# Performance work log

Hardware: AMD Instinct MI355X
Metric: run time of the kernel (lower is better)

The kernel has to match this reference:

```python
import jax, jax.numpy as jnp
import numpy as np

B, S, HID, NH = 2, 2048, 2048, 16
NOPE, ROPE, VD = 128, 64, 128
QKD = NOPE + ROPE          # 192
KVR, QR = 512, 1536
EPS = 1e-6
SCALE = QKD ** (-0.5)


def rmsnorm(x, gamma, eps=EPS):
    return x * jax.lax.rsqrt(jnp.mean(x * x, axis=-1, keepdims=True) + eps) * gamma


def rotate_half(x):
    h = x.shape[-1] // 2
    return jnp.concatenate([-x[..., h:], x[..., :h]], axis=-1)


def apply_rope(x, cos, sin):
    # x: [b, h, s, d_rope]; cos/sin: [b, 1, s, d_rope]
    return x * cos + rotate_half(x) * sin


def setup_inputs() -> dict:
    key = jax.random.key(0)
    ks = jax.random.split(key, 8)
    hidden_states = jax.random.normal(ks[0], (B, S, HID), dtype=jnp.float32)
    # Standard NeoX-style rotary tables for the decoupled RoPE sub-dim
    pos = jnp.arange(S, dtype=jnp.float32)
    inv_freq = 1.0 / (10000.0 ** (jnp.arange(0, ROPE, 2, dtype=jnp.float32) / ROPE))
    freqs = pos[:, None] * inv_freq[None, :]              # [S, ROPE/2]
    emb = jnp.concatenate([freqs, freqs], axis=-1)        # [S, ROPE]
    cos = jnp.broadcast_to(jnp.cos(emb)[None], (B, S, ROPE)).astype(jnp.float32)
    sin = jnp.broadcast_to(jnp.sin(emb)[None], (B, S, ROPE)).astype(jnp.float32)
    std = 0.02
    Wq_down = jax.random.normal(ks[1], (QR, HID), dtype=jnp.float32) * std
    q_gamma = jnp.ones((QR,), dtype=jnp.float32)
    Wq_up = jax.random.normal(ks[2], (NH * QKD, QR), dtype=jnp.float32) * std
    Wkv_down = jax.random.normal(ks[3], (KVR + ROPE, HID), dtype=jnp.float32) * std
    kv_gamma = jnp.ones((KVR,), dtype=jnp.float32)
    Wkv_up = jax.random.normal(ks[4], (NH * (NOPE + VD), KVR), dtype=jnp.float32) * std
    Wo = jax.random.normal(ks[5], (HID, NH * VD), dtype=jnp.float32) * std
    return {
        "hidden_states": hidden_states, "cos": cos, "sin": sin,
        "Wq_down": Wq_down, "q_gamma": q_gamma, "Wq_up": Wq_up,
        "Wkv_down": Wkv_down, "kv_gamma": kv_gamma, "Wkv_up": Wkv_up,
        "Wo": Wo,
    }


def reference(hidden_states, cos, sin, Wq_down, q_gamma, Wq_up,
              Wkv_down, kv_gamma, Wkv_up, Wo):
    b, s, _ = hidden_states.shape
    cos4 = cos[:, None, :, :]  # [b,1,s,ROPE]
    sin4 = sin[:, None, :, :]

    # Q path: low-rank down -> RMSNorm -> up
    q_lat = rmsnorm(hidden_states @ Wq_down.T, q_gamma)            # [b,s,QR]
    q = (q_lat @ Wq_up.T).reshape(b, s, NH, QKD).transpose(0, 2, 1, 3)  # [b,h,s,QKD]
    q_nope, q_rope = q[..., :NOPE], q[..., NOPE:]
    q_rope = apply_rope(q_rope, cos4, sin4)
    q = jnp.concatenate([q_nope, q_rope], axis=-1)                 # [b,h,s,QKD]

    # KV path: joint down-proj -> split latent / shared rope key
    kv = hidden_states @ Wkv_down.T                                # [b,s,KVR+ROPE]
    c_kv, k_rope = kv[..., :KVR], kv[..., KVR:]
    c_kv = rmsnorm(c_kv, kv_gamma)
    kvx = (c_kv @ Wkv_up.T).reshape(b, s, NH, NOPE + VD).transpose(0, 2, 1, 3)
    k_nope, v = kvx[..., :NOPE], kvx[..., NOPE:]                   # [b,h,s,*]

    # Shared rope key, broadcast to all heads, rotated
    k_rope = apply_rope(k_rope[:, None, :, :], cos4, sin4)         # [b,1,s,ROPE]
    k_rope = jnp.broadcast_to(k_rope, (b, NH, s, ROPE))
    k = jnp.concatenate([k_nope, k_rope], axis=-1)                 # [b,h,s,QKD]

    # SDPA with causal mask (V zero-padded to QKD in the original -> identical
    # to using V directly and slicing, so we use V directly)
    scores = jnp.einsum('bhqd,bhkd->bhqk', q, k) * SCALE           # [b,h,s,s]
    causal = jnp.tril(jnp.ones((s, s), dtype=bool))
    scores = jnp.where(causal[None, None], scores, jnp.finfo(scores.dtype).min)
    attn = jax.nn.softmax(scores, axis=-1)
    out = jnp.einsum('bhqk,bhkd->bhqd', attn, v)                   # [b,h,s,VD]
    out = out.transpose(0, 2, 1, 3).reshape(b, s, NH * VD)
    return out @ Wo.T                                              # [b,s,HID]
```

## Files before the change

kernel.cpp:

```cpp
#include <hip/hip_runtime.h>
#include <math.h>

#define SCALE_F 0.0721687836487032f

typedef __attribute__((ext_vector_type(8))) short bf16x8;
typedef __attribute__((ext_vector_type(4))) float f32x4;

static __device__ __forceinline__ short f2bf(float f) {
  unsigned u = __float_as_uint(f);
  u += 0x7fffu + ((u >> 16) & 1u);
  return (short)(u >> 16);
}

static __device__ __forceinline__ void gl_lds16(const void* g, void* l) {
  __builtin_amdgcn_global_load_lds((const __attribute__((address_space(1))) void*)g,
                                   (__attribute__((address_space(3))) void*)l, 16, 0, 0);
}

template <int MODE>
__global__ __launch_bounds__(256) void gemm_mfma(
    const short* __restrict__ A, const short* __restrict__ W,
    void* __restrict__ Cout, int N, int K,
    const float* __restrict__ cosb, const float* __restrict__ sinb,
    short* __restrict__ out2)
{
  __shared__ __align__(16) short As[128 * 32];
  __shared__ __align__(16) short Ws[128 * 32];
  const int tid = threadIdx.x;
  const int lane = tid & 63;
  const int quad = lane >> 4, n16 = lane & 15;
  const int bm = blockIdx.y * 128, bn = blockIdx.x * 128;
  const int wr = ((tid >> 6) >> 1) * 64, wc = ((tid >> 6) & 1) * 64;

  f32x4 acc[4][4];
  #pragma unroll
  for (int i = 0; i < 4; ++i)
    #pragma unroll
    for (int j = 0; j < 4; ++j) acc[i][j] = (f32x4){0.f, 0.f, 0.f, 0.f};

  const int r0 = tid >> 2, c0 = (tid & 3) * 8;
  const short* a0p = A + (size_t)(bm + r0) * K + c0;
  const short* a1p = A + (size_t)(bm + 64 + r0) * K + c0;
  const short* w0p = W + (size_t)(bn + r0) * K + c0;
  const short* w1p = W + (size_t)(bn + 64 + r0) * K + c0;
  short* asd0 = &As[tid * 8];
  short* asd1 = &As[2048 + tid * 8];
  short* wsd0 = &Ws[tid * 8];
  short* wsd1 = &Ws[2048 + tid * 8];

  for (int k0 = 0; k0 < K; k0 += 32) {
    gl_lds16(a0p, asd0);
    gl_lds16(a1p, asd1);
    gl_lds16(w0p, wsd0);
    gl_lds16(w1p, wsd1);
    a0p += 32; a1p += 32; w0p += 32; w1p += 32;
    __syncthreads();

    bf16x8 af[4], wf[4];
    #pragma unroll
    for (int i = 0; i < 4; ++i) {
      af[i] = *(const bf16x8*)&As[(wr + i * 16 + n16) * 32 + quad * 8];
      wf[i] = *(const bf16x8*)&Ws[(wc + i * 16 + n16) * 32 + quad * 8];
    }
    #pragma unroll
    for (int i = 0; i < 4; ++i)
      #pragma unroll
      for (int j = 0; j < 4; ++j)
        acc[i][j] = __builtin_amdgcn_mfma_f32_16x16x32_bf16(af[i], wf[j], acc[i][j], 0, 0, 0);
    __syncthreads();
  }

  if (MODE == 0) {
    #pragma unroll
    for (int i = 0; i < 4; ++i)
      #pragma unroll
      for (int r = 0; r < 4; ++r) {
        size_t row = (size_t)(bm + wr + i * 16 + quad * 4 + r);
        #pragma unroll
        for (int j = 0; j < 4; ++j)
          ((float*)Cout)[row * N + bn + wc + j * 16 + n16] = acc[i][j][r];
      }
  } else if (MODE == 2) {
    #pragma unroll
    for (int i = 0; i < 4; ++i)
      #pragma unroll
      for (int r = 0; r < 4; ++r) {
        int m = bm + wr + i * 16 + quad * 4 + r;
        int bb = m >> 11, s = m & 2047;
        #pragma unroll
        for (int j = 0; j < 4; ++j) {
          int col = bn + wc + j * 16 + n16;
          int h = col / 192, c = col - h * 192;
          float v = acc[i][j][r];
          if (c >= 128) {
            int jr = c - 128;
            float part = acc[i][j ^ 2][r];
            float cs = cosb[(size_t)m * 64 + jr], sn = sinb[(size_t)m * 64 + jr];
            v = (jr < 32) ? (v * cs - part * sn) : (v * cs + part * sn);
          }
          ((short*)Cout)[(((size_t)(bb * 16 + h)) * 2048 + s) * 192 + c] = f2bf(v * SCALE_F);
        }
      }
  } else {
    #pragma unroll
    for (int i = 0; i < 4; ++i)
      #pragma unroll
      for (int r = 0; r < 4; ++r) {
        int m = bm + wr + i * 16 + quad * 4 + r;
        int bb = m >> 11, s = m & 2047;
        #pragma unroll
        for (int j = 0; j < 4; ++j) {
          int col = bn + wc + j * 16 + n16;
          int h = col >> 8, c = col & 255;
          short v = f2bf(acc[i][j][r]);
          if (c < 128)
            ((short*)Cout)[(((size_t)(bb * 16 + h)) * 2048 + s) * 192 + c] = v;
          else
            out2[((size_t)(bb * 16 + h) * 128 + (c - 128)) * 2048 + s] = v;
        }
      }
  }
}

__global__ __launch_bounds__(256) void cast_all(
    const float* __restrict__ hidden, const float* __restrict__ Wqd,
    const float* __restrict__ Wqu, const float* __restrict__ Wkvu,
    const float* __restrict__ Wo, const float* __restrict__ Wkvd,
    short* __restrict__ hb, short* __restrict__ Wqd_b, short* __restrict__ Wqu_b,
    short* __restrict__ Wkvu_b, short* __restrict__ Wo_b, short* __restrict__ Wkvd_b)
{
  int blk = blockIdx.x;
  const float* src; short* dst; int i;
  if (blk < 8192)       { src = hidden; dst = hb;     i = (blk * 256 + threadIdx.x) * 4; }
  else if (blk < 11264) { src = Wqd;  dst = Wqd_b;  i = ((blk - 8192) * 256 + threadIdx.x) * 4; }
  else if (blk < 15872) { src = Wqu;  dst = Wqu_b;  i = ((blk - 11264) * 256 + threadIdx.x) * 4; }
  else if (blk < 17920) { src = Wkvu; dst = Wkvu_b; i = ((blk - 15872) * 256 + threadIdx.x) * 4; }
  else if (blk < 22016) { src = Wo;   dst = Wo_b;   i = ((blk - 17920) * 256 + threadIdx.x) * 4; }
  else {
    i = ((blk - 22016) * 256 + threadIdx.x) * 4;
    int r = i >> 11;
    short4 o = {0, 0, 0, 0};
    if (r < 576) {
      float4 v = *(const float4*)(Wkvd + i);
      o.x = f2bf(v.x); o.y = f2bf(v.y); o.z = f2bf(v.z); o.w = f2bf(v.w);
    }
    *(short4*)(Wkvd_b + i) = o;
    return;
  }
  float4 v = *(const float4*)(src + i);
  short4 o = { f2bf(v.x), f2bf(v.y), f2bf(v.z), f2bf(v.w) };
  *(short4*)(dst + i) = o;
}

__global__ __launch_bounds__(256) void rmsnorm_cast(
    const float* __restrict__ X, const float* __restrict__ gamma,
    short* __restrict__ Y, int C, int sx, int sy)
{
  const float* x = X + (size_t)blockIdx.x * sx;
  short* y = Y + (size_t)blockIdx.x * sy;
  const int tid = threadIdx.x;
  float ss = 0.f;
  for (int c = tid * 4; c < C; c += 1024) {
    float4 v = *(const float4*)(x + c);
    ss += v.x * v.x + v.y * v.y + v.z * v.z + v.w * v.w;
  }
  #pragma unroll
  for (int off = 32; off > 0; off >>= 1) ss += __shfl_down(ss, off, 64);
  __shared__ float red[4];
  if ((tid & 63) == 0) red[tid >> 6] = ss;
  __syncthreads();
  float tot = red[0] + red[1] + red[2] + red[3];
  float scale = rsqrtf(tot / (float)C + 1e-6f);
  for (int c = tid * 4; c < C; c += 1024) {
    float4 v = *(const float4*)(x + c);
    float4 g = *(const float4*)(gamma + c);
    short4 o = { f2bf(v.x * scale * g.x), f2bf(v.y * scale * g.y),
                 f2bf(v.z * scale * g.z), f2bf(v.w * scale * g.w) };
    *(short4*)(y + c) = o;
  }
}

__global__ __launch_bounds__(256) void rmsnorm_kv_rope(
    const float* __restrict__ kvf, const float* __restrict__ gamma,
    const float* __restrict__ cosb, const float* __restrict__ sinb,
    short* __restrict__ ckv, short* __restrict__ kr)
{
  const int m = blockIdx.x;
  const float* x = kvf + (size_t)m * 640;
  short* y = ckv + (size_t)m * 512;
  const int tid = threadIdx.x;
  float ss = 0.f;
  for (int c = tid * 4; c < 512; c += 1024) {
    float4 v = *(const float4*)(x + c);
    ss += v.x * v.x + v.y * v.y + v.z * v.z + v.w * v.w;
  }
  #pragma unroll
  for (int off = 32; off > 0; off >>= 1) ss += __shfl_down(ss, off, 64);
  __shared__ float red[4];
  if ((tid & 63) == 0) red[tid >> 6] = ss;
  __syncthreads();
  float tot = red[0] + red[1] + red[2] + red[3];
  float scale = rsqrtf(tot / 512.f + 1e-6f);
  for (int c = tid * 4; c < 512; c += 1024) {
    float4 v = *(const float4*)(x + c);
    float4 g = *(const float4*)(gamma + c);
    short4 o = { f2bf(v.x * scale * g.x), f2bf(v.y * scale * g.y),
                 f2bf(v.z * scale * g.z), f2bf(v.w * scale * g.w) };
    *(short4*)(y + c) = o;
  }
  if (tid < 32) {
    const float* cb = cosb + (size_t)m * 64;
    const float* sb = sinb + (size_t)m * 64;
    float x1 = x[512 + tid], x2 = x[512 + tid + 32];
    kr[(size_t)m * 64 + tid]      = f2bf(x1 * cb[tid] - x2 * sb[tid]);
    kr[(size_t)m * 64 + tid + 32] = f2bf(x2 * cb[tid + 32] + x1 * sb[tid + 32]);
  }
}

__global__ __launch_bounds__(256) void krope_fill(
    const short* __restrict__ kr, short* __restrict__ Kb)
{
  int m = blockIdx.x;
  int b = m >> 11, s = m & 2047;
  for (int idx = threadIdx.x; idx < 1024; idx += 256) {
    int h = idx >> 6, j = idx & 63;
    Kb[(((size_t)(b * 16 + h)) * 2048 + s) * 192 + 128 + j] = kr[(size_t)m * 64 + j];
  }
}

#define PSTR 72

__global__ __launch_bounds__(256, 1) void flash_mfma(
    const short* __restrict__ Qb, const short* __restrict__ Kb,
    const short* __restrict__ Vt, short* __restrict__ attnb)
{
  __shared__ __align__(16) short KsF[2][24 * 512];
  __shared__ __align__(16) short VsF[2][16 * 512];
  __shared__ __align__(16) short Ps[4][32 * PSTR];

  const int h = blockIdx.x;
  const int pid = blockIdx.y;
  const int b = blockIdx.z;
  const int bh = b * 16 + h;
  const int tid = threadIdx.x;
  const int wave = tid >> 6, lane = tid & 63;
  const int quad = lane >> 4, n16 = lane & 15;
  const int lq = lane >> 2, lr = lane & 3;

  #pragma unroll
  for (int ph = 0; ph < 2; ++ph) {
    const int qt = ph ? pid : (15 - pid);
    const int qw = qt * 128 + wave * 32;
    const int nkt = 2 * qt + 2;

    bf16x8 aQ[2][6];
    #pragma unroll
    for (int rg = 0; rg < 2; ++rg) {
      const short* qp = Qb + ((size_t)bh * 2048 + qw + rg * 16 + n16) * 192 + quad * 8;
      #pragma unroll
      for (int t = 0; t < 6; ++t) aQ[rg][t] = *(const bf16x8*)(qp + t * 32);
    }

    f32x4 O[2][8];
    #pragma unroll
    for (int rg = 0; rg < 2; ++rg)
      #pragma unroll
      for (int i = 0; i < 8; ++i) O[rg][i] = (f32x4){0.f, 0.f, 0.f, 0.f};
    float lp[2][4];
    #pragma unroll
    for (int rg = 0; rg < 2; ++rg)
      #pragma unroll
      for (int r = 0; r < 4; ++r) lp[rg][r] = 0.f;

    short* pw = &Ps[wave][0];

    {
      const short* kbase = Kb + ((size_t)bh * 2048 + wave * 16 + lq) * 192 + lr * 8;
      #pragma unroll
      for (int u = 0; u < 6; ++u)
        gl_lds16(kbase + u * 32, &KsF[0][(wave * 6 + u) * 512 + lane * 8]);
      #pragma unroll
      for (int u = 0; u < 4; ++u) {
        int ci = wave * 4 + u, ks = ci >> 3, vt = ci & 7;
        gl_lds16(Vt + ((size_t)bh * 128 + vt * 16 + lq) * 2048 + ks * 32 + lr * 8,
                 &VsF[0][ci * 512 + lane * 8]);
      }
    }

    for (int kt = 0; kt < nkt; ++kt) {
      __syncthreads();
      const int cur = kt & 1;
      if (kt + 1 < nkt) {
        const int nb = (kt + 1) & 1;
        const short* kbase = Kb + ((size_t)bh * 2048 + (kt + 1) * 64 + wave * 16 + lq) * 192 + lr * 8;
        #pragma unroll
        for (int u = 0; u < 6; ++u)
          gl_lds16(kbase + u * 32, &KsF[nb][(wave * 6 + u) * 512 + lane * 8]);
        #pragma unroll
        for (int u = 0; u < 4; ++u) {
          int ci = wave * 4 + u, ks = ci >> 3, vt = ci & 7;
          gl_lds16(Vt + ((size_t)bh * 128 + vt * 16 + lq) * 2048 + (kt + 1) * 64 + ks * 32 + lr * 8,
                   &VsF[nb][ci * 512 + lane * 8]);
        }
      }

      if (kt * 64 <= qw + 31) {
        float s[2][4][4];
        bool act[4];
        const bool tail = (kt * 64 + 63 > qw);
        #pragma unroll
        for (int ct = 0; ct < 4; ++ct) {
          act[ct] = (kt * 64 + ct * 16 <= qw + 31);
          if (act[ct]) {
            f32x4 acc0 = (f32x4){0.f, 0.f, 0.f, 0.f};
            f32x4 acc1 = (f32x4){0.f, 0.f, 0.f, 0.f};
            #pragma unroll
            for (int t = 0; t < 6; ++t) {
              bf16x8 bk = *(const bf16x8*)&KsF[cur][(ct * 6 + t) * 512 + n16 * 32 + quad * 8];
              acc0 = __builtin_amdgcn_mfma_f32_16x16x32_bf16(aQ[0][t], bk, acc0, 0, 0, 0);
              acc1 = __builtin_amdgcn_mfma_f32_16x16x32_bf16(aQ[1][t], bk, acc1, 0, 0, 0);
            }
            #pragma unroll
            for (int r = 0; r < 4; ++r) { s[0][ct][r] = acc0[r]; s[1][ct][r] = acc1[r]; }
          }
        }

        #pragma unroll
        for (int rg = 0; rg < 2; ++rg)
          #pragma unroll
          for (int ct = 0; ct < 4; ++ct)
            #pragma unroll
            for (int r = 0; r < 4; ++r) {
              float v = 0.f;
              if (act[ct]) {
                v = __expf(s[rg][ct][r]);
                if (tail) {
                  int key = kt * 64 + ct * 16 + n16;
                  if (key > qw + rg * 16 + quad * 4 + r) v = 0.f;
                }
              }
              lp[rg][r] += v;
              pw[(rg * 16 + quad * 4 + r) * PSTR + ct * 16 + n16] = f2bf(v);
            }

        #pragma unroll
        for (int ks = 0; ks < 2; ++ks) {
          if (kt * 64 + ks * 32 <= qw + 31) {
            bf16x8 aP0 = *(const bf16x8*)&pw[(n16) * PSTR + ks * 32 + quad * 8];
            bf16x8 aP1 = *(const bf16x8*)&pw[(16 + n16) * PSTR + ks * 32 + quad * 8];
            #pragma unroll
            for (int vt = 0; vt < 8; ++vt) {
              bf16x8 bV = *(const bf16x8*)&VsF[cur][(ks * 8 + vt) * 512 + n16 * 32 + quad * 8];
              O[0][vt] = __builtin_amdgcn_mfma_f32_16x16x32_bf16(aP0, bV, O[0][vt], 0, 0, 0);
              O[1][vt] = __builtin_amdgcn_mfma_f32_16x16x32_bf16(aP1, bV, O[1][vt], 0, 0, 0);
            }
          }
        }
      }
    }

    #pragma unroll
    for (int rg = 0; rg < 2; ++rg) {
      float inv_l[4];
      #pragma unroll
      for (int r = 0; r < 4; ++r) {
        float l = lp[rg][r];
        l += __shfl_xor(l, 1);
        l += __shfl_xor(l, 2);
        l += __shfl_xor(l, 4);
        l += __shfl_xor(l, 8);
        inv_l[r] = 1.f / l;
      }
      #pragma unroll
      for (int vt = 0; vt < 8; ++vt)
        #pragma unroll
        for (int r = 0; r < 4; ++r) {
          size_t m = (size_t)b * 2048 + qw + rg * 16 + quad * 4 + r;
          attnb[(m * 16 + h) * 128 + vt * 16 + n16] = f2bf(O[rg][vt][r] * inv_l[r]);
        }
    }
    __syncthreads();
  }
}

extern "C" void kernel_launch(void* const* d_in, const int* in_sizes, int n_in,
                              void* d_out, int out_size, void* d_ws, size_t ws_size,
                              hipStream_t stream)
{
  const float* hidden   = (const float*)d_in[0];
  const float* cosb     = (const float*)d_in[1];
  const float* sinb     = (const float*)d_in[2];
  const float* Wq_down  = (const float*)d_in[3];
  const float* q_gamma  = (const float*)d_in[4];
  const float* Wq_up    = (const float*)d_in[5];
  const float* Wkv_down = (const float*)d_in[6];
  const float* kv_gamma = (const float*)d_in[7];
  const float* Wkv_up   = (const float*)d_in[8];
  const float* Wo       = (const float*)d_in[9];
  float* out = (float*)d_out;

  char* base = (char*)d_ws;
  short* hb  = (short*)base;
  float* kvf = (float*)(base + 16777216);
  short* Qb  = (short*)base;
  char* pB = base + 27262976;
  short* Wqd_b  = (short*)pB;
  short* Wkvd_b = (short*)(pB + 6291456);
  short* Wqu_b  = (short*)(pB + 8912896);
  short* Wkvu_b = (short*)(pB + 18350080);
  short* Wo_b   = (short*)(pB + 22544384);
  char* pC = pB + 30932992;
  float* q_lat = (float*)pC;
  short* Kb    = (short*)pC;
  char* pD = pC + 25165824;
  short* q_lat_b = (short*)pD;
  short* ckv_b   = (short*)(pD + 12582912);
  short* krope_b = (short*)(pD + 16777216);
  short* attn_b  = (short*)pD;
  char* pE = pD + 17301504;
  short* Vt = (short*)pE;

  dim3 blk(256);

  cast_all<<<23296, blk, 0, stream>>>(hidden, Wq_down, Wq_up, Wkv_up, Wo, Wkv_down,
                                      hb, Wqd_b, Wqu_b, Wkvu_b, Wo_b, Wkvd_b);

  gemm_mfma<0><<<dim3(12, 32), blk, 0, stream>>>(hb, Wqd_b, q_lat, 1536, 2048, nullptr, nullptr, nullptr);
  gemm_mfma<0><<<dim3(5, 32), blk, 0, stream>>>(hb, Wkvd_b, kvf, 640, 2048, nullptr, nullptr, nullptr);

  rmsnorm_cast<<<4096, blk, 0, stream>>>(q_lat, q_gamma, q_lat_b, 1536, 1536, 1536);
  rmsnorm_kv_rope<<<4096, blk, 0, stream>>>(kvf, kv_gamma, cosb, sinb, ckv_b, krope_b);

  gemm_mfma<2><<<dim3(24, 32), blk, 0, stream>>>(q_lat_b, Wqu_b, Qb, 3072, 1536, cosb, sinb, nullptr);
  gemm_mfma<3><<<dim3(32, 32), blk, 0, stream>>>(ckv_b, Wkvu_b, Kb, 4096, 512, nullptr, nullptr, Vt);
  krope_fill<<<4096, blk, 0, stream>>>(krope_b, Kb);

  flash_mfma<<<dim3(16, 8, 2), blk, 0, stream>>>(Qb, Kb, Vt, attn_b);
  gemm_mfma<0><<<dim3(16, 32), blk, 0, stream>>>(attn_b, Wo_b, out, 2048, 2048, nullptr, nullptr, nullptr);
}
```

Measured before the change: 556.3 us.

## Restructure flash attention to one q-tile per block with two-block occupancy

The flash kernel stops pairing two causal q-tiles per block. It now launches one q-tile per block, with heavy tiles scheduled first, and drops the K/V double buffer so two blocks can share a CU. The QK^T MFMA operands are swapped, so each lane holds a column of keys for one query. That allows packed 4-wide P stores to LDS and a cheaper row-sum reduction across quads. The cost is that loads are no longer prefetched, so latency must be hidden by the second resident block instead, and load balancing now depends on the hardware scheduler.

After: 541.8 us. 2.6% less time.

```diff
diff --git a/kernel.cpp b/kernel.cpp
--- a/kernel.cpp
+++ b/kernel.cpp
@@ -5,6 +5,7 @@
 
 typedef __attribute__((ext_vector_type(8))) short bf16x8;
 typedef __attribute__((ext_vector_type(4))) float f32x4;
+typedef __attribute__((ext_vector_type(4))) unsigned short u16x4;
 
 static __device__ __forceinline__ short f2bf(float f) {
   unsigned u = __float_as_uint(f);
@@ -230,156 +231,134 @@
 
 #define PSTR 72
 
-__global__ __launch_bounds__(256, 1) void flash_mfma(
+__global__ __launch_bounds__(256, 2) void flash_mfma(
     const short* __restrict__ Qb, const short* __restrict__ Kb,
     const short* __restrict__ Vt, short* __restrict__ attnb)
 {
-  __shared__ __align__(16) short KsF[2][24 * 512];
-  __shared__ __align__(16) short VsF[2][16 * 512];
+  __shared__ __align__(16) short KsF[24 * 512];
+  __shared__ __align__(16) short VsF[16 * 512];
   __shared__ __align__(16) short Ps[4][32 * PSTR];
 
   const int h = blockIdx.x;
-  const int pid = blockIdx.y;
+  const int qt = (gridDim.y - 1) - blockIdx.y;
   const int b = blockIdx.z;
   const int bh = b * 16 + h;
   const int tid = threadIdx.x;
   const int wave = tid >> 6, lane = tid & 63;
   const int quad = lane >> 4, n16 = lane & 15;
   const int lq = lane >> 2, lr = lane & 3;
-
-  #pragma unroll
-  for (int ph = 0; ph < 2; ++ph) {
-    const int qt = ph ? pid : (15 - pid);
-    const int qw = qt * 128 + wave * 32;
-    const int nkt = 2 * qt + 2;
-
-    bf16x8 aQ[2][6];
-    #pragma unroll
-    for (int rg = 0; rg < 2; ++rg) {
-      const short* qp = Qb + ((size_t)bh * 2048 + qw + rg * 16 + n16) * 192 + quad * 8;
-      #pragma unroll
-      for (int t = 0; t < 6; ++t) aQ[rg][t] = *(const bf16x8*)(qp + t * 32);
-    }
-
-    f32x4 O[2][8];
-    #pragma unroll
-    for (int rg = 0; rg < 2; ++rg)
-      #pragma unroll
-      for (int i = 0; i < 8; ++i) O[rg][i] = (f32x4){0.f, 0.f, 0.f, 0.f};
-    float lp[2][4];
-    #pragma unroll
-    for (int rg = 0; rg < 2; ++rg)
-      #pragma unroll
-      for (int r = 0; r < 4; ++r) lp[rg][r] = 0.f;
-
-    short* pw = &Ps[wave][0];
-
+  const int qw = qt * 128 + wave * 32;
+  const int nkt = 2 * qt + 2;
+
+  bf16x8 aQ[2][6];
+  #pragma unroll
+  for (int rg = 0; rg < 2; ++rg) {
+    const short* qp = Qb + ((size_t)bh * 2048 + qw + rg * 16 + n16) * 192 + quad * 8;
+    #pragma unroll
+    for (int t = 0; t < 6; ++t) aQ[rg][t] = *(const bf16x8*)(qp + t * 32);
+  }
+
+  f32x4 O[2][8];
+  #pragma unroll
+  for (int rg = 0; rg < 2; ++rg)
+    #pragma unroll
+    for (int i = 0; i < 8; ++i) O[rg][i] = (f32x4){0.f, 0.f, 0.f, 0.f};
+  float lp[2] = {0.f, 0.f};
+
+  short* pw = &Ps[wave][0];
+
+  for (int kt = 0; kt < nkt; ++kt) {
     {
-      const short* kbase = Kb + ((size_t)bh * 2048 + wave * 16 + lq) * 192 + lr * 8;
+      const short* kbase = Kb + ((size_t)bh * 2048 + kt * 64 + wave * 16 + lq) * 192 + lr * 8;
       #pragma unroll
       for (int u = 0; u < 6; ++u)
-        gl_lds16(kbase + u * 32, &KsF[0][(wave * 6 + u) * 512 + lane * 8]);
+        gl_lds16(kbase + u * 32, &KsF[(wave * 6 + u) * 512 + lane * 8]);
       #pragma unroll
       for (int u = 0; u < 4; ++u) {
         int ci = wave * 4 + u, ks = ci >> 3, vt = ci & 7;
-        gl_lds16(Vt + ((size_t)bh * 128 + vt * 16 + lq) * 2048 + ks * 32 + lr * 8,
-                 &VsF[0][ci * 512 + lane * 8]);
+        gl_lds16(Vt + ((size_t)bh * 128 + vt * 16 + lq) * 2048 + kt * 64 + ks * 32 + lr * 8,
+                 &VsF[ci * 512 + lane * 8]);
       }
     }
-
-    for (int kt = 0; kt < nkt; ++kt) {
-      __syncthreads();
-      const int cur = kt & 1;
-      if (kt + 1 < nkt) {
-        const int nb = (kt + 1) & 1;
-        const short* kbase = Kb + ((size_t)bh * 2048 + (kt + 1) * 64 + wave * 16 + lq) * 192 + lr * 8;
-        #pragma unroll
-        for (int u = 0; u < 6; ++u)
-          gl_lds16(kbase + u * 32, &KsF[nb][(wave * 6 + u) * 512 + lane * 8]);
-        #pragma unroll
-        for (int u = 0; u < 4; ++u) {
-          int ci = wave * 4 + u, ks = ci >> 3, vt = ci & 7;
-          gl_lds16(Vt + ((size_t)bh * 128 + vt * 16 + lq) * 2048 + (kt + 1) * 64 + ks * 32 + lr * 8,
-                   &VsF[nb][ci * 512 + lane * 8]);
+    __syncthreads();
+
+    if (kt * 64 <= qw + 31) {
+      float s[4][2][4];
+      bool act[4];
+      const bool tail = (kt * 64 + 63 > qw);
+      #pragma unroll
+      for (int ct = 0; ct < 4; ++ct) {
+        act[ct] = (kt * 64 + ct * 16 <= qw + 31);
+        if (act[ct]) {
+          f32x4 a0 = (f32x4){0.f, 0.f, 0.f, 0.f};
+          f32x4 a1 = (f32x4){0.f, 0.f, 0.f, 0.f};
+          #pragma unroll
+          for (int t = 0; t < 6; ++t) {
+            bf16x8 ak = *(const bf16x8*)&KsF[(ct * 6 + t) * 512 + n16 * 32 + quad * 8];
+            a0 = __builtin_amdgcn_mfma_f32_16x16x32_bf16(ak, aQ[0][t], a0, 0, 0, 0);
+            a1 = __builtin_amdgcn_mfma_f32_16x16x32_bf16(ak, aQ[1][t], a1, 0, 0, 0);
+          }
+          #pragma unroll
+          for (int r = 0; r < 4; ++r) { s[ct][0][r] = a0[r]; s[ct][1][r] = a1[r]; }
         }
       }
 
-      if (kt * 64 <= qw + 31) {
-        float s[2][4][4];
-        bool act[4];
-        const bool tail = (kt * 64 + 63 > qw);
+      #pragma unroll
+      for (int rg = 0; rg < 2; ++rg) {
+        const int q = qw + rg * 16 + n16;
         #pragma unroll
         for (int ct = 0; ct < 4; ++ct) {
-          act[ct] = (kt * 64 + ct * 16 <= qw + 31);
-          if (act[ct]) {
-            f32x4 acc0 = (f32x4){0.f, 0.f, 0.f, 0.f};
-            f32x4 acc1 = (f32x4){0.f, 0.f, 0.f, 0.f};
-            #pragma unroll
-            for (int t = 0; t < 6; ++t) {
-              bf16x8 bk = *(const bf16x8*)&KsF[cur][(ct * 6 + t) * 512 + n16 * 32 + quad * 8];
-              acc0 = __builtin_amdgcn_mfma_f32_16x16x32_bf16(aQ[0][t], bk, acc0, 0, 0, 0);
-              acc1 = __builtin_amdgcn_mfma_f32_16x16x32_bf16(aQ[1][t], bk, acc1, 0, 0, 0);
+          u16x4 pk;
+          #pragma unroll
+          for (int r = 0; r < 4; ++r) {
+            float v = 0.f;
+            if (act[ct]) {
+              v = __expf(s[ct][rg][r]);
+              if (tail) {
+                int key = kt * 64 + ct * 16 + quad * 4 + r;
+                if (key > q) v = 0.f;
+              }
             }
-            #pragma unroll
-            for (int r = 0; r < 4; ++r) { s[0][ct][r] = acc0[r]; s[1][ct][r] = acc1[r]; }
+            lp[rg] += v;
+            pk[r] = (unsigned short)f2bf(v);
+          }
+          *(u16x4*)&pw[(rg * 16 + n16) * PSTR + ct * 16 + quad * 4] = pk;
+        }
+      }
+
+      #pragma unroll
+      for (int ks = 0; ks < 2; ++ks) {
+        if (kt * 64 + ks * 32 <= qw + 31) {
+          bf16x8 aP0 = *(const bf16x8*)&pw[(n16) * PSTR + ks * 32 + quad * 8];
+          bf16x8 aP1 = *(const bf16x8*)&pw[(16 + n16) * PSTR + ks * 32 + quad * 8];
+          #pragma unroll
+          for (int vt = 0; vt < 8; ++vt) {
+            bf16x8 bV = *(const bf16x8*)&VsF[(ks * 8 + vt) * 512 + n16 * 32 + quad * 8];
+            O[0][vt] = __builtin_amdgcn_mfma_f32_16x16x32_bf16(aP0, bV, O[0][vt], 0, 0, 0);
+            O[1][vt] = __builtin_amdgcn_mfma_f32_16x16x32_bf16(aP1, bV, O[1][vt], 0, 0, 0);
           }
         }
-
-        #pragma unroll
-        for (int rg = 0; rg < 2; ++rg)
-          #pragma unroll
-          for (int ct = 0; ct < 4; ++ct)
-            #pragma unroll
-            for (int r = 0; r < 4; ++r) {
-              float v = 0.f;
-              if (act[ct]) {
-                v = __expf(s[rg][ct][r]);
-                if (tail) {
-                  int key = kt * 64 + ct * 16 + n16;
-                  if (key > qw + rg * 16 + quad * 4 + r) v = 0.f;
-                }
-              }
-              lp[rg][r] += v;
-              pw[(rg * 16 + quad * 4 + r) * PSTR + ct * 16 + n16] = f2bf(v);
-            }
-
-        #pragma unroll
-        for (int ks = 0; ks < 2; ++ks) {
-          if (kt * 64 + ks * 32 <= qw + 31) {
-            bf16x8 aP0 = *(const bf16x8*)&pw[(n16) * PSTR + ks * 32 + quad * 8];
-            bf16x8 aP1 = *(const bf16x8*)&pw[(16 + n16) * PSTR + ks * 32 + quad * 8];
-            #pragma unroll
-            for (int vt = 0; vt < 8; ++vt) {
-              bf16x8 bV = *(const bf16x8*)&VsF[cur][(ks * 8 + vt) * 512 + n16 * 32 + quad * 8];
-              O[0][vt] = __builtin_amdgcn_mfma_f32_16x16x32_bf16(aP0, bV, O[0][vt], 0, 0, 0);
-              O[1][vt] = __builtin_amdgcn_mfma_f32_16x16x32_bf16(aP1, bV, O[1][vt], 0, 0, 0);
-            }
-          }
-        }
-      }
-    }
-
-    #pragma unroll
-    for (int rg = 0; rg < 2; ++rg) {
-      float inv_l[4];
-      #pragma unroll
-      for (int r = 0; r < 4; ++r) {
-        float l = lp[rg][r];
-        l += __shfl_xor(l, 1);
-        l += __shfl_xor(l, 2);
-        l += __shfl_xor(l, 4);
-        l += __shfl_xor(l, 8);
-        inv_l[r] = 1.f / l;
-      }
-      #pragma unroll
-      for (int vt = 0; vt < 8; ++vt)
-        #pragma unroll
-        for (int r = 0; r < 4; ++r) {
-          size_t m = (size_t)b * 2048 + qw + rg * 16 + quad * 4 + r;
-          attnb[(m * 16 + h) * 128 + vt * 16 + n16] = f2bf(O[rg][vt][r] * inv_l[r]);
-        }
+      }
     }
     __syncthreads();
+  }
+
+  #pragma unroll
+  for (int rg = 0; rg < 2; ++rg) {
+    float l = lp[rg];
+    l += __shfl_xor(l, 16);
+    l += __shfl_xor(l, 32);
+    float inv_l[4];
+    #pragma unroll
+    for (int r = 0; r < 4; ++r)
+      inv_l[r] = 1.f / __shfl(l, quad * 4 + r);
+    #pragma unroll
+    for (int vt = 0; vt < 8; ++vt)
+      #pragma unroll
+      for (int r = 0; r < 4; ++r) {
+        size_t m = (size_t)b * 2048 + qw + rg * 16 + quad * 4 + r;
+        attnb[(m * 16 + h) * 128 + vt * 16 + n16] = f2bf(O[rg][vt][r] * inv_l[r]);
+      }
   }
 }
 
@@ -435,6 +414,6 @@
   gemm_mfma<3><<<dim3(32, 32), blk, 0, stream>>>(ckv_b, Wkvu_b, Kb, 4096, 512, nullptr, nullptr, Vt);
   krope_fill<<<4096, blk, 0, stream>>>(krope_b, Kb);
 
-  flash_mfma<<<dim3(16, 8, 2), blk, 0, stream>>>(Qb, Kb, Vt, attn_b);
+  flash_mfma<<<dim3(16, 16, 2), blk, 0, stream>>>(Qb, Kb, Vt, attn_b);
   gemm_mfma<0><<<dim3(16, 32), blk, 0, stream>>>(attn_b, Wo_b, out, 2048, 2048, nullptr, nullptr, nullptr);
 }
```
